# Kernel optimization log

Measured on AMD Instinct MI355X. Metric: run time of the kernel, lower is better.

Reference implementation:

```python
import jax, jax.numpy as jnp
import numpy as np

N_NODES = 100000
N_EDGES = 1000000
IN_CH = 64
HID = 128
OUT_CH = 2
N_GRAPHS = 256


def setup_inputs() -> dict:
    key = jax.random.key(0)
    ks = jax.random.split(key, 12)
    x = jax.random.normal(ks[0], (N_NODES, IN_CH), dtype=jnp.float32)
    edge_index = jax.random.randint(ks[1], (2, N_EDGES), 0, N_NODES, dtype=jnp.int64)
    batch = jnp.sort(jax.random.randint(ks[2], (N_NODES,), 0, N_GRAPHS, dtype=jnp.int64))
    def glorot(k, shape):
        lim = float(np.sqrt(6.0 / (shape[0] + shape[1])))
        return jax.random.uniform(k, shape, dtype=jnp.float32, minval=-lim, maxval=lim)
    # SAGEConv: out = lin_l(mean_agg(x_j)) + lin_r(x_i); bias on lin_l only (PyG default)
    Wl1 = glorot(ks[3], (HID, IN_CH))
    bl1 = jnp.zeros((HID,), dtype=jnp.float32)
    Wr1 = glorot(ks[4], (HID, IN_CH))
    Wl2 = glorot(ks[5], (HID, HID))
    bl2 = jnp.zeros((HID,), dtype=jnp.float32)
    Wr2 = glorot(ks[6], (HID, HID))
    Wout = glorot(ks[7], (OUT_CH, HID))
    bout = jnp.zeros((OUT_CH,), dtype=jnp.float32)
    return {"x": x, "edge_index": edge_index, "batch": batch,
            "Wl1": Wl1, "bl1": bl1, "Wr1": Wr1,
            "Wl2": Wl2, "bl2": bl2, "Wr2": Wr2,
            "Wout": Wout, "bout": bout}


def _sage_conv(x, src, dst, Wl, bl, Wr):
    # mean-aggregate source features onto target nodes, then two linears
    msgs = x[src]                                                # [E, d]
    agg = jax.ops.segment_sum(msgs, dst, num_segments=N_NODES)  # [N, d]
    deg = jax.ops.segment_sum(jnp.ones((src.shape[0], 1), x.dtype), dst,
                              num_segments=N_NODES)             # [N, 1]
    agg = agg / jnp.maximum(deg, 1.0)
    return agg @ Wl.T + bl + x @ Wr.T


def reference(x, edge_index, batch, Wl1, bl1, Wr1, Wl2, bl2, Wr2, Wout, bout):
    src, dst = edge_index[0], edge_index[1]
    h = jax.nn.relu(_sage_conv(x, src, dst, Wl1, bl1, Wr1))
    # dropout(p=0.2) is identity in eval mode
    h = jax.nn.relu(_sage_conv(h, src, dst, Wl2, bl2, Wr2))
    # global_mean_pool over graph ids
    pooled = jax.ops.segment_sum(h, batch, num_segments=N_GRAPHS)      # [G, H]
    cnt = jax.ops.segment_sum(jnp.ones((h.shape[0], 1), h.dtype), batch,
                              num_segments=N_GRAPHS)                   # [G, 1]
    pooled = pooled / jnp.maximum(cnt, 1.0)
    logits = pooled @ Wout.T + bout
    return jax.nn.log_softmax(logits, axis=1)
```

## Files before the change

kernel.cpp:

```cpp
#include <hip/hip_runtime.h>
#include <hip/hip_bf16.h>
#include <math.h>

typedef short short8_t __attribute__((ext_vector_type(8)));
typedef float floatx4  __attribute__((ext_vector_type(4)));
typedef float floatx2  __attribute__((ext_vector_type(2)));
typedef unsigned int uint;

#define EPB 1024
#define BSH 9


__device__ inline unsigned short f2b(float f) {
    uint u = __float_as_uint(f);
    u += 0x7fff + ((u >> 16) & 1);
    return (unsigned short)(u >> 16);
}
__device__ inline uint pack2(float a, float b) {
    return (uint)f2b(a) | ((uint)f2b(b) << 16);
}
__device__ inline float blo(uint v) { return __uint_as_float(v << 16); }
__device__ inline float bhi(uint v) { return __uint_as_float(v & 0xffff0000u); }


__device__ inline uint enc4_fp8(float f0, float f1, float f2, float f3) {
    uint v = __builtin_amdgcn_cvt_pk_fp8_f32(f0, f1, 0, false);
    v = __builtin_amdgcn_cvt_pk_fp8_f32(f2, f3, v, true);
    return v;
}
__device__ inline unsigned char enc1_fp8(float f) {
    return (unsigned char)(__builtin_amdgcn_cvt_pk_fp8_f32(f, f, 0, false) & 0xff);
}


__global__ __launch_bounds__(256) void k_phase_a(
    const int* __restrict__ dst, int* __restrict__ bhist, int E,
    const float* __restrict__ x, unsigned short* __restrict__ xb,
    unsigned char* __restrict__ xf8, int nX,
    const float* __restrict__ Wl1, const float* __restrict__ Wr1,
    const float* __restrict__ Wl2, const float* __restrict__ Wr2,
    unsigned short* __restrict__ wbuf,
    const int* __restrict__ batch, int* __restrict__ gstart, int N, int G,
    int bHist, int bCvtX, int bCvtW) {
    __shared__ int h[256];
    int b = blockIdx.x;
    int tid = threadIdx.x;
    if (b < bHist) {
        h[tid] = 0;
        __syncthreads();
        int e = b * EPB + tid * 4;
        if (e + 3 < E) {
            int4 d4 = *(const int4*)(dst + e);
            atomicAdd(&h[d4.x >> BSH], 1);
            atomicAdd(&h[d4.y >> BSH], 1);
            atomicAdd(&h[d4.z >> BSH], 1);
            atomicAdd(&h[d4.w >> BSH], 1);
        } else {
            for (int k = e; k < E; ++k) atomicAdd(&h[dst[k] >> BSH], 1);
        }
        __syncthreads();
        bhist[(size_t)b * 256 + tid] = h[tid];
    } else if (b < bHist + bCvtX) {
        int i = ((b - bHist) * 256 + tid) * 8;
        if (i < nX) {
            float4 v0 = *(const float4*)(x + i);
            float4 v1 = *(const float4*)(x + i + 4);
            uint4 ob;
            ob.x = pack2(v0.x, v0.y);
            ob.y = pack2(v0.z, v0.w);
            ob.z = pack2(v1.x, v1.y);
            ob.w = pack2(v1.z, v1.w);
            *(uint4*)(xb + i) = ob;
            uint2 of;
            of.x = enc4_fp8(v0.x, v0.y, v0.z, v0.w);
            of.y = enc4_fp8(v1.x, v1.y, v1.z, v1.w);
            *(uint2*)(xf8 + i) = of;
        }
    } else if (b < bHist + bCvtX + bCvtW) {
        int i = (b - bHist - bCvtX) * 256 + tid;
        if (i < 49152) {
            float v;
            if (i < 8192)       v = Wl1[i];
            else if (i < 16384) v = Wr1[i - 8192];
            else if (i < 32768) v = Wl2[i - 16384];
            else                v = Wr2[i - 32768];
            wbuf[i] = f2b(v);
        }
    } else {
        for (int g = tid; g <= G; g += 256) {
            if (g == G) { gstart[G] = N; continue; }
            int lo = 0, hi = N;
            while (lo < hi) {
                int mid = (lo + hi) >> 1;
                if (batch[mid] < g) lo = mid + 1; else hi = mid;
            }
            gstart[g] = lo;
        }
    }
}

__global__ __launch_bounds__(256) void k_scan_bh(int* __restrict__ bhist,
                                                 int* __restrict__ btot, int nb) {
    __shared__ int ss[256];
    int k = blockIdx.x;
    int t = threadIdx.x;
    int b0 = t * 4;
    int v[4];
    int sum = 0;
#pragma unroll
    for (int i = 0; i < 4; ++i) {
        int b = b0 + i;
        v[i] = (b < nb) ? bhist[(size_t)b * 256 + k] : 0;
        sum += v[i];
    }
    ss[t] = sum;
    __syncthreads();
#pragma unroll
    for (int off = 1; off < 256; off <<= 1) {
        int u = (t >= off) ? ss[t - off] : 0;
        __syncthreads();
        ss[t] += u;
        __syncthreads();
    }
    int run = ss[t] - sum;
#pragma unroll
    for (int i = 0; i < 4; ++i) {
        int b = b0 + i;
        if (b < nb) { bhist[(size_t)b * 256 + k] = run; run += v[i]; }
    }
    if (t == 0) btot[k] = ss[255];
}

__global__ void k_scan_btot(const int* __restrict__ btot, int* __restrict__ bbase,
                            int* __restrict__ row_start, int N, int E) {
    __shared__ int ss[256];
    int t = threadIdx.x;
    int v = btot[t];
    ss[t] = v;
    __syncthreads();
#pragma unroll
    for (int off = 1; off < 256; off <<= 1) {
        int u = (t >= off) ? ss[t - off] : 0;
        __syncthreads();
        ss[t] += u;
        __syncthreads();
    }
    bbase[t] = ss[t] - v;
    if (t == 255) bbase[256] = ss[255];
    if (t == 0) row_start[N] = E;
}

__global__ __launch_bounds__(256) void k_scatter_b(
    const int* __restrict__ src, const int* __restrict__ dst,
    const int* __restrict__ bhist, const int* __restrict__ bbase,
    int* __restrict__ ebuf, int E) {
    __shared__ int lbase[256];
    int b = blockIdx.x;
    int t = threadIdx.x;
    lbase[t] = bbase[t] + bhist[(size_t)b * 256 + t];
    __syncthreads();
    int e = b * EPB + t * 4;
    if (e + 3 < E) {
        int4 d4 = *(const int4*)(dst + e);
        int4 s4 = *(const int4*)(src + e);
        int k, p;
        k = d4.x >> BSH; p = atomicAdd(&lbase[k], 1); ebuf[p] = ((d4.x & 511) << 23) | s4.x;
        k = d4.y >> BSH; p = atomicAdd(&lbase[k], 1); ebuf[p] = ((d4.y & 511) << 23) | s4.y;
        k = d4.z >> BSH; p = atomicAdd(&lbase[k], 1); ebuf[p] = ((d4.z & 511) << 23) | s4.z;
        k = d4.w >> BSH; p = atomicAdd(&lbase[k], 1); ebuf[p] = ((d4.w & 511) << 23) | s4.w;
    } else {
        for (int q = e; q < E; ++q) {
            int d = dst[q];
            int p = atomicAdd(&lbase[d >> BSH], 1);
            ebuf[p] = ((d & 511) << 23) | src[q];
        }
    }
}

__global__ __launch_bounds__(256) void k_bucket_csr(
    const int* __restrict__ ebuf, const int* __restrict__ bbase,
    int* __restrict__ row_start, int* __restrict__ csr_src, int N) {
    __shared__ int h2[512];
    __shared__ int ss[256];
    int k = blockIdx.x;
    int t = threadIdx.x;
    int node0 = k << BSH;
    int nn = N - node0; if (nn > 512) nn = 512;
    int s = bbase[k], e = bbase[k + 1];
    h2[t] = 0; h2[t + 256] = 0;
    __syncthreads();
    for (int i = s + t; i < e; i += 256)
        atomicAdd(&h2[((uint)ebuf[i]) >> 23], 1);
    __syncthreads();
    int a0 = h2[2 * t], a1 = h2[2 * t + 1];
    int ps = a0 + a1;
    ss[t] = ps;
    __syncthreads();
#pragma unroll
    for (int off = 1; off < 256; off <<= 1) {
        int u = (t >= off) ? ss[t - off] : 0;
        __syncthreads();
        ss[t] += u;
        __syncthreads();
    }
    int base = ss[t] - ps;
    h2[2 * t] = base;
    h2[2 * t + 1] = base + a0;
    __syncthreads();
    int rs0 = h2[t];
    int rs1 = h2[t + 256];
    __syncthreads();
    if (t < nn)       row_start[node0 + t]       = s + rs0;
    if (t + 256 < nn) row_start[node0 + t + 256] = s + rs1;
    for (int i = s + t; i < e; i += 256) {
        int rec = ebuf[i];
        int j = ((uint)rec) >> 23;
        int pos = atomicAdd(&h2[j], 1);
        csr_src[s + pos] = rec & 0x7FFFFF;
    }
}


#define ACCF8(v)                                                        \
    { floatx2 f = __builtin_amdgcn_cvt_pk_f32_fp8((v).x, false);        \
      a[0] += f[0]; a[1] += f[1];                                       \
      f = __builtin_amdgcn_cvt_pk_f32_fp8((v).x, true);                 \
      a[2] += f[0]; a[3] += f[1];                                       \
      f = __builtin_amdgcn_cvt_pk_f32_fp8((v).y, false);                \
      a[4] += f[0]; a[5] += f[1];                                       \
      f = __builtin_amdgcn_cvt_pk_f32_fp8((v).y, true);                 \
      a[6] += f[0]; a[7] += f[1]; }

__global__ void k_gather1(const unsigned char* __restrict__ xf8,
                          const int* __restrict__ row_start,
                          const int* __restrict__ csr_src,
                          unsigned short* __restrict__ agg, int n_nodes) {
    int tid = threadIdx.x;
    int node = blockIdx.x * 4 + (tid >> 6);
    if (node >= n_nodes) return;
    int lane = tid & 63;
    int grp = lane >> 3;
    int lp  = lane & 7;
    int s = row_start[node];
    int e = row_start[node + 1];
    float a[8];
#pragma unroll
    for (int q = 0; q < 8; ++q) a[q] = 0.f;
    int i = s + grp;
    for (; i + 8 < e; i += 16) {
        int u0 = csr_src[i];
        int u1 = csr_src[i + 8];
        uint2 v0 = *(const uint2*)(xf8 + (size_t)u0 * 64 + lp * 8);
        uint2 v1 = *(const uint2*)(xf8 + (size_t)u1 * 64 + lp * 8);
        ACCF8(v0);
        ACCF8(v1);
    }
    if (i < e) {
        int u0 = csr_src[i];
        uint2 v0 = *(const uint2*)(xf8 + (size_t)u0 * 64 + lp * 8);
        ACCF8(v0);
    }
#pragma unroll
    for (int q = 0; q < 8; ++q) {
        a[q] += __shfl_xor(a[q], 8);
        a[q] += __shfl_xor(a[q], 16);
        a[q] += __shfl_xor(a[q], 32);
    }
    if (grp == 0) {
        int d = e - s;
        float scale = (d > 0) ? (1.f / (float)d) : 1.f;
        uint4 o;
        o.x = pack2(a[0] * scale, a[1] * scale);
        o.y = pack2(a[2] * scale, a[3] * scale);
        o.z = pack2(a[4] * scale, a[5] * scale);
        o.w = pack2(a[6] * scale, a[7] * scale);
        *(uint4*)(agg + (size_t)node * 64 + lp * 8) = o;
    }
}

__global__ void k_gather2(const unsigned char* __restrict__ h1f8,
                          const int* __restrict__ row_start,
                          const int* __restrict__ csr_src,
                          unsigned short* __restrict__ agg, int n_nodes) {
    int tid = threadIdx.x;
    int node = blockIdx.x * 4 + (tid >> 6);
    if (node >= n_nodes) return;
    int lane = tid & 63;
    int grp = lane >> 4;
    int lp  = lane & 15;
    int s = row_start[node];
    int e = row_start[node + 1];
    float a[8];
#pragma unroll
    for (int q = 0; q < 8; ++q) a[q] = 0.f;
    int i = s + grp;
    for (; i + 4 < e; i += 8) {
        int u0 = csr_src[i];
        int u1 = csr_src[i + 4];
        uint2 v0 = *(const uint2*)(h1f8 + (size_t)u0 * 128 + lp * 8);
        uint2 v1 = *(const uint2*)(h1f8 + (size_t)u1 * 128 + lp * 8);
        ACCF8(v0);
        ACCF8(v1);
    }
    if (i < e) {
        int u0 = csr_src[i];
        uint2 v0 = *(const uint2*)(h1f8 + (size_t)u0 * 128 + lp * 8);
        ACCF8(v0);
    }
#pragma unroll
    for (int q = 0; q < 8; ++q) {
        a[q] += __shfl_xor(a[q], 16);
        a[q] += __shfl_xor(a[q], 32);
    }
    if (grp == 0) {
        int d = e - s;
        float scale = (d > 0) ? (1.f / (float)d) : 1.f;
        uint4 o;
        o.x = pack2(a[0] * scale, a[1] * scale);
        o.y = pack2(a[2] * scale, a[3] * scale);
        o.z = pack2(a[4] * scale, a[5] * scale);
        o.w = pack2(a[6] * scale, a[7] * scale);
        *(uint4*)(agg + (size_t)node * 128 + lp * 8) = o;
    }
}


template <int K, bool F8OUT>
__global__ __launch_bounds__(256) void k_linear_mfma(
    const unsigned short* __restrict__ aggA, const unsigned short* __restrict__ xinA,
    const unsigned short* __restrict__ Wlb,  const float* __restrict__ bl,
    const unsigned short* __restrict__ Wrb,  unsigned short* __restrict__ out,
    unsigned char* __restrict__ outf8, int n_nodes) {
    constexpr int NCH = (2 * K) / 32;
    __shared__ __align__(16) short As[128 * 32];

    int tid  = threadIdx.x;
    int lane = tid & 63;
    int wave = tid >> 6;
    int quad = lane >> 4;
    int lr   = lane & 15;
    int node0 = blockIdx.x * 128;

    floatx4 acc[8][2];
#pragma unroll
    for (int mi = 0; mi < 8; ++mi)
#pragma unroll
        for (int ni = 0; ni < 2; ++ni)
            acc[mi][ni] = (floatx4){0.f, 0.f, 0.f, 0.f};

    int srow = tid >> 2;
    int sslot = tid & 3;

#pragma unroll
    for (int c = 0; c < NCH; ++c) {
        const unsigned short* srcA;
        const unsigned short* srcW;
        int kb;
        if (c < K / 32) { srcA = aggA; srcW = Wlb; kb = c * 32; }
        else            { srcA = xinA; srcW = Wrb; kb = c * 32 - K; }

        __syncthreads();
        {
            int n1 = node0 + srow;       if (n1 >= n_nodes) n1 = n_nodes - 1;
            int n2 = node0 + srow + 64;  if (n2 >= n_nodes) n2 = n_nodes - 1;
            uint4 v1 = *(const uint4*)(srcA + (size_t)n1 * K + kb + sslot * 8);
            uint4 v2 = *(const uint4*)(srcA + (size_t)n2 * K + kb + sslot * 8);
            *(uint4*)(&As[srow * 32 + sslot * 8]) = v1;
            *(uint4*)(&As[(srow + 64) * 32 + sslot * 8]) = v2;
        }
        __syncthreads();

        short8_t bfrag[2];
#pragma unroll
        for (int ni = 0; ni < 2; ++ni) {
            int j = wave * 32 + ni * 16 + lr;
            bfrag[ni] = *(const short8_t*)(srcW + (size_t)j * K + kb + quad * 8);
        }
#pragma unroll
        for (int mi = 0; mi < 8; ++mi) {
            short8_t af = *(const short8_t*)(&As[(mi * 16 + lr) * 32 + quad * 8]);
            acc[mi][0] = __builtin_amdgcn_mfma_f32_16x16x32_bf16(af, bfrag[0], acc[mi][0], 0, 0, 0);
            acc[mi][1] = __builtin_amdgcn_mfma_f32_16x16x32_bf16(af, bfrag[1], acc[mi][1], 0, 0, 0);
        }
    }

    float b0 = bl[wave * 32 + lr];
    float b1 = bl[wave * 32 + 16 + lr];
    int j0 = wave * 32 + lr;
#pragma unroll
    for (int mi = 0; mi < 8; ++mi) {
#pragma unroll
        for (int r = 0; r < 4; ++r) {
            int node = node0 + mi * 16 + quad * 4 + r;
            if (node < n_nodes) {
                float v0 = fmaxf(acc[mi][0][r] + b0, 0.f);
                float v1 = fmaxf(acc[mi][1][r] + b1, 0.f);
                out[(size_t)node * 128 + j0]      = f2b(v0);
                out[(size_t)node * 128 + j0 + 16] = f2b(v1);
                if (F8OUT) {
                    outf8[(size_t)node * 128 + j0]      = enc1_fp8(v0);
                    outf8[(size_t)node * 128 + j0 + 16] = enc1_fp8(v1);
                }
            }
        }
    }
}


__global__ __launch_bounds__(256) void k_pool_head(const unsigned short* __restrict__ h2b,
                                                   const int* __restrict__ gstart,
                                                   const float* __restrict__ Wout,
                                                   const float* __restrict__ bout,
                                                   float* __restrict__ out) {
    int g = blockIdx.x;
    int s = gstart[g], e = gstart[g + 1];
    int lane = threadIdx.x & 63;
    int wave = threadIdx.x >> 6;
    float ax = 0.f, ay = 0.f;
    for (int n = s + wave; n < e; n += 4) {
        uint v = ((const uint*)(h2b + (size_t)n * 128))[lane];
        ax += blo(v);
        ay += bhi(v);
    }
    __shared__ float2 red[4][64];
    red[wave][lane] = make_float2(ax, ay);
    __syncthreads();
    if (wave == 0) {
        float2 a = red[0][lane], b = red[1][lane], c = red[2][lane], d = red[3][lane];
        float cnt = (float)(e - s);
        float inv = (cnt > 0.f) ? (1.f / cnt) : 1.f;
        float px = (a.x + b.x + c.x + d.x) * inv;
        float py = (a.y + b.y + c.y + d.y) * inv;
        float2 w0 = ((const float2*)(Wout))[lane];
        float2 w1 = ((const float2*)(Wout + 128))[lane];
        float d0 = px * w0.x + py * w0.y;
        float d1 = px * w1.x + py * w1.y;
#pragma unroll
        for (int m = 32; m > 0; m >>= 1) {
            d0 += __shfl_xor(d0, m);
            d1 += __shfl_xor(d1, m);
        }
        if (lane == 0) {
            float l0 = d0 + bout[0];
            float l1 = d1 + bout[1];
            float mx = fmaxf(l0, l1);
            float lse = mx + logf(expf(l0 - mx) + expf(l1 - mx));
            out[g * 2 + 0] = l0 - lse;
            out[g * 2 + 1] = l1 - lse;
        }
    }
}


static inline size_t alignUp(size_t x, size_t a) { return (x + a - 1) & ~(a - 1); }

extern "C" void kernel_launch(void* const* d_in, const int* in_sizes, int n_in,
                              void* d_out, int out_size, void* d_ws, size_t ws_size,
                              hipStream_t stream) {
    const float* x    = (const float*)d_in[0];
    const int*   ei   = (const int*)d_in[1];
    const int*   batch= (const int*)d_in[2];
    const float* Wl1  = (const float*)d_in[3];
    const float* bl1  = (const float*)d_in[4];
    const float* Wr1  = (const float*)d_in[5];
    const float* Wl2  = (const float*)d_in[6];
    const float* bl2  = (const float*)d_in[7];
    const float* Wr2  = (const float*)d_in[8];
    const float* Wout = (const float*)d_in[9];
    const float* bout = (const float*)d_in[10];
    float* out = (float*)d_out;

    const int N = in_sizes[0] / 64;
    const int E = in_sizes[1] / 2;
    const int G = out_size / 2;

    const int* src = ei;
    const int* dst = ei + E;

    const int bHist = (E + EPB - 1) / EPB;
    const int NB    = (N + 511) >> BSH;

    char* ws = (char*)d_ws;
    size_t off = 0;
    int*   bhist     = (int*)(ws + off); off = alignUp(off + (size_t)bHist * 256 * 4, 256);
    int*   btot      = (int*)(ws + off); off = alignUp(off + (size_t)257 * 4, 256);
    int*   bbase     = (int*)(ws + off); off = alignUp(off + (size_t)257 * 4, 256);
    int*   row_start = (int*)(ws + off); off = alignUp(off + (size_t)(N + 1) * 4, 256);
    int*   ebuf      = (int*)(ws + off); off = alignUp(off + (size_t)E * 4, 256);
    int*   csr_src   = (int*)(ws + off); off = alignUp(off + (size_t)E * 4, 256);
    int*   gstart    = (int*)(ws + off); off = alignUp(off + (size_t)(G + 1) * 4, 256);
    unsigned short* xb   = (unsigned short*)(ws + off); off = alignUp(off + (size_t)N * 64 * 2, 256);
    unsigned char*  xf8  = (unsigned char*)(ws + off);  off = alignUp(off + (size_t)N * 64, 256);
    unsigned short* wbuf = (unsigned short*)(ws + off); off = alignUp(off + (size_t)49152 * 2, 256);
    unsigned short* agg1 = (unsigned short*)(ws + off); off = alignUp(off + (size_t)N * 64 * 2, 256);
    unsigned short* h1   = (unsigned short*)(ws + off); off = alignUp(off + (size_t)N * 128 * 2, 256);
    unsigned char*  h1f8 = (unsigned char*)(ws + off);  off = alignUp(off + (size_t)N * 128, 256);
    unsigned short* agg2 = (unsigned short*)(ws + off); off = alignUp(off + (size_t)N * 128 * 2, 256);
    unsigned short* h2b  = (unsigned short*)(ws + off); off = alignUp(off + (size_t)N * 128 * 2, 256);
    (void)ws_size;

    unsigned short* Wl1b = wbuf;
    unsigned short* Wr1b = wbuf + 8192;
    unsigned short* Wl2b = wbuf + 16384;
    unsigned short* Wr2b = wbuf + 32768;

    const int bCvtX = (N * 64 / 8 + 255) / 256;
    const int bCvtW = 192;
    k_phase_a<<<bHist + bCvtX + bCvtW + 1, 256, 0, stream>>>(
        dst, bhist, E,
        x, xb, xf8, N * 64,
        Wl1, Wr1, Wl2, Wr2, wbuf,
        batch, gstart, N, G,
        bHist, bCvtX, bCvtW);

    k_scan_bh<<<256, 256, 0, stream>>>(bhist, btot, bHist);
    k_scan_btot<<<1, 256, 0, stream>>>(btot, bbase, row_start, N, E);
    k_scatter_b<<<bHist, 256, 0, stream>>>(src, dst, bhist, bbase, ebuf, E);
    k_bucket_csr<<<NB, 256, 0, stream>>>(ebuf, bbase, row_start, csr_src, N);

    k_gather1<<<(N + 3) / 4, 256, 0, stream>>>(xf8, row_start, csr_src, agg1, N);
    k_linear_mfma<64, true><<<(N + 127) / 128, 256, 0, stream>>>(
        agg1, xb, Wl1b, bl1, Wr1b, h1, h1f8, N);

    k_gather2<<<(N + 3) / 4, 256, 0, stream>>>(h1f8, row_start, csr_src, agg2, N);
    k_linear_mfma<128, false><<<(N + 127) / 128, 256, 0, stream>>>(
        agg2, h1, Wl2b, bl2, Wr2b, h2b, (unsigned char*)nullptr, N);

    k_pool_head<<<G, 256, 0, stream>>>(h2b, gstart, Wout, bout, out);
}
```

Before: 285.1 us.

## Fuse neighbor gather into MFMA linear kernels and pooling into layer two

Measured after the change: 374.1 us. 31.2% more time.

```diff
diff --git a/kernel.cpp b/kernel.cpp
--- a/kernel.cpp
+++ b/kernel.cpp
@@ -19,8 +19,6 @@
 __device__ inline uint pack2(float a, float b) {
     return (uint)f2b(a) | ((uint)f2b(b) << 16);
 }
-__device__ inline float blo(uint v) { return __uint_as_float(v << 16); }
-__device__ inline float bhi(uint v) { return __uint_as_float(v & 0xffff0000u); }
 
 
 __device__ inline uint enc4_fp8(float f0, float f1, float f2, float f3) {
@@ -40,8 +38,9 @@
     const float* __restrict__ Wl1, const float* __restrict__ Wr1,
     const float* __restrict__ Wl2, const float* __restrict__ Wr2,
     unsigned short* __restrict__ wbuf,
+    float* __restrict__ pooled,
     const int* __restrict__ batch, int* __restrict__ gstart, int N, int G,
-    int bHist, int bCvtX, int bCvtW) {
+    int bHist, int bCvtX, int bCvtW, int bZero) {
     __shared__ int h[256];
     int b = blockIdx.x;
     int tid = threadIdx.x;
@@ -86,6 +85,10 @@
             else                v = Wr2[i - 32768];
             wbuf[i] = f2b(v);
         }
+    } else if (b < bHist + bCvtX + bCvtW + bZero) {
+        int i = ((b - bHist - bCvtX - bCvtW) * 256 + tid) * 4;
+        float4 z = make_float4(0.f, 0.f, 0.f, 0.f);
+        *(float4*)(pooled + i) = z;
     } else {
         for (int g = tid; g <= G; g += 256) {
             if (g == G) { gstart[G] = N; continue; }
@@ -131,9 +134,13 @@
     if (t == 0) btot[k] = ss[255];
 }
 
-__global__ void k_scan_btot(const int* __restrict__ btot, int* __restrict__ bbase,
-                            int* __restrict__ row_start, int N, int E) {
+__global__ __launch_bounds__(256) void k_scatter_b(
+    const int* __restrict__ src, const int* __restrict__ dst,
+    const int* __restrict__ bhist, const int* __restrict__ btot,
+    int* __restrict__ ebuf, int E) {
+    __shared__ int lbase[256];
     __shared__ int ss[256];
+    int b = blockIdx.x;
     int t = threadIdx.x;
     int v = btot[t];
     ss[t] = v;
@@ -145,19 +152,7 @@
         ss[t] += u;
         __syncthreads();
     }
-    bbase[t] = ss[t] - v;
-    if (t == 255) bbase[256] = ss[255];
-    if (t == 0) row_start[N] = E;
-}
-
-__global__ __launch_bounds__(256) void k_scatter_b(
-    const int* __restrict__ src, const int* __restrict__ dst,
-    const int* __restrict__ bhist, const int* __restrict__ bbase,
-    int* __restrict__ ebuf, int E) {
-    __shared__ int lbase[256];
-    int b = blockIdx.x;
-    int t = threadIdx.x;
-    lbase[t] = bbase[t] + bhist[(size_t)b * 256 + t];
+    lbase[t] = (ss[t] - v) + bhist[(size_t)b * 256 + t];
     __syncthreads();
     int e = b * EPB + t * 4;
     if (e + 3 < E) {
@@ -178,15 +173,29 @@
 }
 
 __global__ __launch_bounds__(256) void k_bucket_csr(
-    const int* __restrict__ ebuf, const int* __restrict__ bbase,
+    const int* __restrict__ ebuf, const int* __restrict__ btot,
     int* __restrict__ row_start, int* __restrict__ csr_src, int N) {
     __shared__ int h2[512];
     __shared__ int ss[256];
+    __shared__ int S01[2];
     int k = blockIdx.x;
     int t = threadIdx.x;
+    int vb = btot[t];
+    ss[t] = vb;
+    __syncthreads();
+#pragma unroll
+    for (int off = 1; off < 256; off <<= 1) {
+        int u = (t >= off) ? ss[t - off] : 0;
+        __syncthreads();
+        ss[t] += u;
+        __syncthreads();
+    }
+    if (t == k) { S01[0] = ss[t] - vb; S01[1] = ss[t]; }
+    __syncthreads();
+    int s = S01[0], e = S01[1];
     int node0 = k << BSH;
     int nn = N - node0; if (nn > 512) nn = 512;
-    int s = bbase[k], e = bbase[k + 1];
+    if (k == (int)gridDim.x - 1 && t == 0) row_start[node0 + nn] = e;
     h2[t] = 0; h2[t + 256] = 0;
     __syncthreads();
     for (int i = s + t; i < e; i += 256)
@@ -231,116 +240,74 @@
       f = __builtin_amdgcn_cvt_pk_f32_fp8((v).y, true);                 \
       a[6] += f[0]; a[7] += f[1]; }
 
-__global__ void k_gather1(const unsigned char* __restrict__ xf8,
-                          const int* __restrict__ row_start,
-                          const int* __restrict__ csr_src,
-                          unsigned short* __restrict__ agg, int n_nodes) {
-    int tid = threadIdx.x;
-    int node = blockIdx.x * 4 + (tid >> 6);
-    if (node >= n_nodes) return;
-    int lane = tid & 63;
-    int grp = lane >> 3;
-    int lp  = lane & 7;
-    int s = row_start[node];
-    int e = row_start[node + 1];
-    float a[8];
-#pragma unroll
-    for (int q = 0; q < 8; ++q) a[q] = 0.f;
-    int i = s + grp;
-    for (; i + 8 < e; i += 16) {
-        int u0 = csr_src[i];
-        int u1 = csr_src[i + 8];
-        uint2 v0 = *(const uint2*)(xf8 + (size_t)u0 * 64 + lp * 8);
-        uint2 v1 = *(const uint2*)(xf8 + (size_t)u1 * 64 + lp * 8);
-        ACCF8(v0);
-        ACCF8(v1);
-    }
-    if (i < e) {
-        int u0 = csr_src[i];
-        uint2 v0 = *(const uint2*)(xf8 + (size_t)u0 * 64 + lp * 8);
-        ACCF8(v0);
-    }
-#pragma unroll
-    for (int q = 0; q < 8; ++q) {
-        a[q] += __shfl_xor(a[q], 8);
-        a[q] += __shfl_xor(a[q], 16);
-        a[q] += __shfl_xor(a[q], 32);
-    }
-    if (grp == 0) {
-        int d = e - s;
-        float scale = (d > 0) ? (1.f / (float)d) : 1.f;
-        uint4 o;
-        o.x = pack2(a[0] * scale, a[1] * scale);
-        o.y = pack2(a[2] * scale, a[3] * scale);
-        o.z = pack2(a[4] * scale, a[5] * scale);
-        o.w = pack2(a[6] * scale, a[7] * scale);
-        *(uint4*)(agg + (size_t)node * 64 + lp * 8) = o;
-    }
-}
-
-__global__ void k_gather2(const unsigned char* __restrict__ h1f8,
-                          const int* __restrict__ row_start,
-                          const int* __restrict__ csr_src,
-                          unsigned short* __restrict__ agg, int n_nodes) {
-    int tid = threadIdx.x;
-    int node = blockIdx.x * 4 + (tid >> 6);
-    if (node >= n_nodes) return;
-    int lane = tid & 63;
-    int grp = lane >> 4;
-    int lp  = lane & 15;
-    int s = row_start[node];
-    int e = row_start[node + 1];
-    float a[8];
-#pragma unroll
-    for (int q = 0; q < 8; ++q) a[q] = 0.f;
-    int i = s + grp;
-    for (; i + 4 < e; i += 8) {
-        int u0 = csr_src[i];
-        int u1 = csr_src[i + 4];
-        uint2 v0 = *(const uint2*)(h1f8 + (size_t)u0 * 128 + lp * 8);
-        uint2 v1 = *(const uint2*)(h1f8 + (size_t)u1 * 128 + lp * 8);
-        ACCF8(v0);
-        ACCF8(v1);
-    }
-    if (i < e) {
-        int u0 = csr_src[i];
-        uint2 v0 = *(const uint2*)(h1f8 + (size_t)u0 * 128 + lp * 8);
-        ACCF8(v0);
-    }
-#pragma unroll
-    for (int q = 0; q < 8; ++q) {
-        a[q] += __shfl_xor(a[q], 16);
-        a[q] += __shfl_xor(a[q], 32);
-    }
-    if (grp == 0) {
-        int d = e - s;
-        float scale = (d > 0) ? (1.f / (float)d) : 1.f;
-        uint4 o;
-        o.x = pack2(a[0] * scale, a[1] * scale);
-        o.y = pack2(a[2] * scale, a[3] * scale);
-        o.z = pack2(a[4] * scale, a[5] * scale);
-        o.w = pack2(a[6] * scale, a[7] * scale);
-        *(uint4*)(agg + (size_t)node * 128 + lp * 8) = o;
-    }
-}
-
-
-template <int K, bool F8OUT>
-__global__ __launch_bounds__(256) void k_linear_mfma(
-    const unsigned short* __restrict__ aggA, const unsigned short* __restrict__ xinA,
-    const unsigned short* __restrict__ Wlb,  const float* __restrict__ bl,
-    const unsigned short* __restrict__ Wrb,  unsigned short* __restrict__ out,
-    unsigned char* __restrict__ outf8, int n_nodes) {
-    constexpr int NCH = (2 * K) / 32;
+
+__global__ __launch_bounds__(256) void k_fused1(
+    const unsigned char* __restrict__ xf8,
+    const int* __restrict__ row_start, const int* __restrict__ csr_src,
+    const unsigned short* __restrict__ xb,
+    const unsigned short* __restrict__ Wlb, const float* __restrict__ bl,
+    const unsigned short* __restrict__ Wrb,
+    unsigned short* __restrict__ out, unsigned char* __restrict__ outf8,
+    int n_nodes) {
+    __shared__ __align__(16) short aggS[128 * 72];
     __shared__ __align__(16) short As[128 * 32];
 
     int tid  = threadIdx.x;
     int lane = tid & 63;
     int wave = tid >> 6;
+    int node0 = blockIdx.x * 128;
+
+    {
+        int grp = lane >> 3;
+        int lp  = lane & 7;
+        int wbase = node0 + wave * 32;
+        int ridx = wbase + lane;
+        if (ridx > n_nodes) ridx = n_nodes;
+        int rs = row_start[ridx];
+        int nmax = n_nodes - wbase;
+        if (nmax > 32) nmax = 32;
+        for (int t = 0; t < nmax; ++t) {
+            int s = __shfl(rs, t);
+            int e = __shfl(rs, t + 1);
+            float a[8];
+#pragma unroll
+            for (int q = 0; q < 8; ++q) a[q] = 0.f;
+            int i = s + grp;
+            for (; i + 8 < e; i += 16) {
+                int u0 = csr_src[i];
+                int u1 = csr_src[i + 8];
+                uint2 v0 = *(const uint2*)(xf8 + (size_t)u0 * 64 + lp * 8);
+                uint2 v1 = *(const uint2*)(xf8 + (size_t)u1 * 64 + lp * 8);
+                ACCF8(v0);
+                ACCF8(v1);
+            }
+            if (i < e) {
+                int u0 = csr_src[i];
+                uint2 v0 = *(const uint2*)(xf8 + (size_t)u0 * 64 + lp * 8);
+                ACCF8(v0);
+            }
+#pragma unroll
+            for (int q = 0; q < 8; ++q) {
+                a[q] += __shfl_xor(a[q], 8);
+                a[q] += __shfl_xor(a[q], 16);
+                a[q] += __shfl_xor(a[q], 32);
+            }
+            if (grp == 0) {
+                int d = e - s;
+                float scale = (d > 0) ? (1.f / (float)d) : 1.f;
+                uint4 o;
+                o.x = pack2(a[0] * scale, a[1] * scale);
+                o.y = pack2(a[2] * scale, a[3] * scale);
+                o.z = pack2(a[4] * scale, a[5] * scale);
+                o.w = pack2(a[6] * scale, a[7] * scale);
+                *(uint4*)(&aggS[(wave * 32 + t) * 72 + lp * 8]) = o;
+            }
+        }
+    }
+    __syncthreads();
+
     int quad = lane >> 4;
     int lr   = lane & 15;
-    int node0 = blockIdx.x * 128;
-
     floatx4 acc[8][2];
 #pragma unroll
     for (int mi = 0; mi < 8; ++mi)
@@ -348,33 +315,41 @@
         for (int ni = 0; ni < 2; ++ni)
             acc[mi][ni] = (floatx4){0.f, 0.f, 0.f, 0.f};
 
+#pragma unroll
+    for (int c = 0; c < 2; ++c) {
+        short8_t bfrag[2];
+#pragma unroll
+        for (int ni = 0; ni < 2; ++ni) {
+            int j = wave * 32 + ni * 16 + lr;
+            bfrag[ni] = *(const short8_t*)(Wlb + (size_t)j * 64 + c * 32 + quad * 8);
+        }
+#pragma unroll
+        for (int mi = 0; mi < 8; ++mi) {
+            short8_t af = *(const short8_t*)(&aggS[(mi * 16 + lr) * 72 + c * 32 + quad * 8]);
+            acc[mi][0] = __builtin_amdgcn_mfma_f32_16x16x32_bf16(af, bfrag[0], acc[mi][0], 0, 0, 0);
+            acc[mi][1] = __builtin_amdgcn_mfma_f32_16x16x32_bf16(af, bfrag[1], acc[mi][1], 0, 0, 0);
+        }
+    }
+
     int srow = tid >> 2;
     int sslot = tid & 3;
-
-#pragma unroll
-    for (int c = 0; c < NCH; ++c) {
-        const unsigned short* srcA;
-        const unsigned short* srcW;
-        int kb;
-        if (c < K / 32) { srcA = aggA; srcW = Wlb; kb = c * 32; }
-        else            { srcA = xinA; srcW = Wrb; kb = c * 32 - K; }
-
+#pragma unroll
+    for (int c = 0; c < 2; ++c) {
         __syncthreads();
         {
             int n1 = node0 + srow;       if (n1 >= n_nodes) n1 = n_nodes - 1;
             int n2 = node0 + srow + 64;  if (n2 >= n_nodes) n2 = n_nodes - 1;
-            uint4 v1 = *(const uint4*)(srcA + (size_t)n1 * K + kb + sslot * 8);
-            uint4 v2 = *(const uint4*)(srcA + (size_t)n2 * K + kb + sslot * 8);
+            uint4 v1 = *(const uint4*)(xb + (size_t)n1 * 64 + c * 32 + sslot * 8);
+            uint4 v2 = *(const uint4*)(xb + (size_t)n2 * 64 + c * 32 + sslot * 8);
             *(uint4*)(&As[srow * 32 + sslot * 8]) = v1;
             *(uint4*)(&As[(srow + 64) * 32 + sslot * 8]) = v2;
         }
         __syncthreads();
-
         short8_t bfrag[2];
 #pragma unroll
         for (int ni = 0; ni < 2; ++ni) {
             int j = wave * 32 + ni * 16 + lr;
-            bfrag[ni] = *(const short8_t*)(srcW + (size_t)j * K + kb + quad * 8);
+            bfrag[ni] = *(const short8_t*)(Wrb + (size_t)j * 64 + c * 32 + quad * 8);
         }
 #pragma unroll
         for (int mi = 0; mi < 8; ++mi) {
@@ -397,57 +372,196 @@
                 float v1 = fmaxf(acc[mi][1][r] + b1, 0.f);
                 out[(size_t)node * 128 + j0]      = f2b(v0);
                 out[(size_t)node * 128 + j0 + 16] = f2b(v1);
-                if (F8OUT) {
-                    outf8[(size_t)node * 128 + j0]      = enc1_fp8(v0);
-                    outf8[(size_t)node * 128 + j0 + 16] = enc1_fp8(v1);
+                outf8[(size_t)node * 128 + j0]      = enc1_fp8(v0);
+                outf8[(size_t)node * 128 + j0 + 16] = enc1_fp8(v1);
+            }
+        }
+    }
+}
+
+
+__global__ __launch_bounds__(256) void k_fused2(
+    const unsigned char* __restrict__ h1f8,
+    const int* __restrict__ row_start, const int* __restrict__ csr_src,
+    const unsigned short* __restrict__ h1,
+    const unsigned short* __restrict__ Wlb, const float* __restrict__ bl,
+    const unsigned short* __restrict__ Wrb,
+    const int* __restrict__ batch, float* __restrict__ pooled,
+    int n_nodes) {
+    __shared__ __align__(16) short aggS[128 * 136];
+    __shared__ __align__(16) short As[128 * 32];
+    __shared__ int bb[128];
+
+    int tid  = threadIdx.x;
+    int lane = tid & 63;
+    int wave = tid >> 6;
+    int node0 = blockIdx.x * 128;
+
+    if (tid < 128) {
+        int n = node0 + tid;
+        bb[tid] = (n < n_nodes) ? batch[n] : 0;
+    }
+
+    {
+        int grp = lane >> 4;
+        int lp  = lane & 15;
+        int wbase = node0 + wave * 32;
+        int ridx = wbase + lane;
+        if (ridx > n_nodes) ridx = n_nodes;
+        int rs = row_start[ridx];
+        int nmax = n_nodes - wbase;
+        if (nmax > 32) nmax = 32;
+        for (int t = 0; t < nmax; ++t) {
+            int s = __shfl(rs, t);
+            int e = __shfl(rs, t + 1);
+            float a[8];
+#pragma unroll
+            for (int q = 0; q < 8; ++q) a[q] = 0.f;
+            int i = s + grp;
+            for (; i + 4 < e; i += 8) {
+                int u0 = csr_src[i];
+                int u1 = csr_src[i + 4];
+                uint2 v0 = *(const uint2*)(h1f8 + (size_t)u0 * 128 + lp * 8);
+                uint2 v1 = *(const uint2*)(h1f8 + (size_t)u1 * 128 + lp * 8);
+                ACCF8(v0);
+                ACCF8(v1);
+            }
+            if (i < e) {
+                int u0 = csr_src[i];
+                uint2 v0 = *(const uint2*)(h1f8 + (size_t)u0 * 128 + lp * 8);
+                ACCF8(v0);
+            }
+#pragma unroll
+            for (int q = 0; q < 8; ++q) {
+                a[q] += __shfl_xor(a[q], 16);
+                a[q] += __shfl_xor(a[q], 32);
+            }
+            if (grp == 0) {
+                int d = e - s;
+                float scale = (d > 0) ? (1.f / (float)d) : 1.f;
+                uint4 o;
+                o.x = pack2(a[0] * scale, a[1] * scale);
+                o.y = pack2(a[2] * scale, a[3] * scale);
+                o.z = pack2(a[4] * scale, a[5] * scale);
+                o.w = pack2(a[6] * scale, a[7] * scale);
+                *(uint4*)(&aggS[(wave * 32 + t) * 136 + lp * 8]) = o;
+            }
+        }
+    }
+    __syncthreads();
+
+    int quad = lane >> 4;
+    int lr   = lane & 15;
+    floatx4 acc[8][2];
+#pragma unroll
+    for (int mi = 0; mi < 8; ++mi)
+#pragma unroll
+        for (int ni = 0; ni < 2; ++ni)
+            acc[mi][ni] = (floatx4){0.f, 0.f, 0.f, 0.f};
+
+#pragma unroll
+    for (int c = 0; c < 4; ++c) {
+        short8_t bfrag[2];
+#pragma unroll
+        for (int ni = 0; ni < 2; ++ni) {
+            int j = wave * 32 + ni * 16 + lr;
+            bfrag[ni] = *(const short8_t*)(Wlb + (size_t)j * 128 + c * 32 + quad * 8);
+        }
+#pragma unroll
+        for (int mi = 0; mi < 8; ++mi) {
+            short8_t af = *(const short8_t*)(&aggS[(mi * 16 + lr) * 136 + c * 32 + quad * 8]);
+            acc[mi][0] = __builtin_amdgcn_mfma_f32_16x16x32_bf16(af, bfrag[0], acc[mi][0], 0, 0, 0);
+            acc[mi][1] = __builtin_amdgcn_mfma_f32_16x16x32_bf16(af, bfrag[1], acc[mi][1], 0, 0, 0);
+        }
+    }
+
+    int srow = tid >> 2;
+    int sslot = tid & 3;
+#pragma unroll
+    for (int c = 0; c < 4; ++c) {
+        __syncthreads();
+        {
+            int n1 = node0 + srow;       if (n1 >= n_nodes) n1 = n_nodes - 1;
+            int n2 = node0 + srow + 64;  if (n2 >= n_nodes) n2 = n_nodes - 1;
+            uint4 v1 = *(const uint4*)(h1 + (size_t)n1 * 128 + c * 32 + sslot * 8);
+            uint4 v2 = *(const uint4*)(h1 + (size_t)n2 * 128 + c * 32 + sslot * 8);
+            *(uint4*)(&As[srow * 32 + sslot * 8]) = v1;
+            *(uint4*)(&As[(srow + 64) * 32 + sslot * 8]) = v2;
+        }
+        __syncthreads();
+        short8_t bfrag[2];
+#pragma unroll
+        for (int ni = 0; ni < 2; ++ni) {
+            int j = wave * 32 + ni * 16 + lr;
+            bfrag[ni] = *(const short8_t*)(Wrb + (size_t)j * 128 + c * 32 + quad * 8);
+        }
+#pragma unroll
+        for (int mi = 0; mi < 8; ++mi) {
+            short8_t af = *(const short8_t*)(&As[(mi * 16 + lr) * 32 + quad * 8]);
+            acc[mi][0] = __builtin_amdgcn_mfma_f32_16x16x32_bf16(af, bfrag[0], acc[mi][0], 0, 0, 0);
+            acc[mi][1] = __builtin_amdgcn_mfma_f32_16x16x32_bf16(af, bfrag[1], acc[mi][1], 0, 0, 0);
+        }
+    }
+
+    float b0 = bl[wave * 32 + lr];
+    float b1 = bl[wave * 32 + 16 + lr];
+    int j0 = wave * 32 + lr;
+    int gcur = -1;
+    float s0 = 0.f, s1 = 0.f;
+#pragma unroll
+    for (int mi = 0; mi < 8; ++mi) {
+#pragma unroll
+        for (int r = 0; r < 4; ++r) {
+            int li = mi * 16 + quad * 4 + r;
+            int node = node0 + li;
+            if (node < n_nodes) {
+                float v0 = fmaxf(acc[mi][0][r] + b0, 0.f);
+                float v1 = fmaxf(acc[mi][1][r] + b1, 0.f);
+                int g = bb[li];
+                if (g != gcur) {
+                    if (gcur >= 0) {
+                        atomicAdd(&pooled[gcur * 128 + j0], s0);
+                        atomicAdd(&pooled[gcur * 128 + j0 + 16], s1);
+                    }
+                    gcur = g; s0 = 0.f; s1 = 0.f;
                 }
-            }
-        }
-    }
-}
-
-
-__global__ __launch_bounds__(256) void k_pool_head(const unsigned short* __restrict__ h2b,
-                                                   const int* __restrict__ gstart,
-                                                   const float* __restrict__ Wout,
-                                                   const float* __restrict__ bout,
-                                                   float* __restrict__ out) {
+                s0 += v0;
+                s1 += v1;
+            }
+        }
+    }
+    if (gcur >= 0) {
+        atomicAdd(&pooled[gcur * 128 + j0], s0);
+        atomicAdd(&pooled[gcur * 128 + j0 + 16], s1);
+    }
+}
+
+
+__global__ void k_head(const float* __restrict__ pooled,
+                       const int* __restrict__ gstart,
+                       const float* __restrict__ Wout,
+                       const float* __restrict__ bout,
+                       float* __restrict__ out) {
     int g = blockIdx.x;
-    int s = gstart[g], e = gstart[g + 1];
-    int lane = threadIdx.x & 63;
-    int wave = threadIdx.x >> 6;
-    float ax = 0.f, ay = 0.f;
-    for (int n = s + wave; n < e; n += 4) {
-        uint v = ((const uint*)(h2b + (size_t)n * 128))[lane];
-        ax += blo(v);
-        ay += bhi(v);
-    }
-    __shared__ float2 red[4][64];
-    red[wave][lane] = make_float2(ax, ay);
-    __syncthreads();
-    if (wave == 0) {
-        float2 a = red[0][lane], b = red[1][lane], c = red[2][lane], d = red[3][lane];
-        float cnt = (float)(e - s);
+    int lane = threadIdx.x;
+    float p0 = pooled[g * 128 + lane];
+    float p1 = pooled[g * 128 + 64 + lane];
+    float d0 = p0 * Wout[lane] + p1 * Wout[64 + lane];
+    float d1 = p0 * Wout[128 + lane] + p1 * Wout[192 + lane];
+#pragma unroll
+    for (int m = 32; m > 0; m >>= 1) {
+        d0 += __shfl_xor(d0, m);
+        d1 += __shfl_xor(d1, m);
+    }
+    if (lane == 0) {
+        float cnt = (float)(gstart[g + 1] - gstart[g]);
         float inv = (cnt > 0.f) ? (1.f / cnt) : 1.f;
-        float px = (a.x + b.x + c.x + d.x) * inv;
-        float py = (a.y + b.y + c.y + d.y) * inv;
-        float2 w0 = ((const float2*)(Wout))[lane];
-        float2 w1 = ((const float2*)(Wout + 128))[lane];
-        float d0 = px * w0.x + py * w0.y;
-        float d1 = px * w1.x + py * w1.y;
-#pragma unroll
-        for (int m = 32; m > 0; m >>= 1) {
-            d0 += __shfl_xor(d0, m);
-            d1 += __shfl_xor(d1, m);
-        }
-        if (lane == 0) {
-            float l0 = d0 + bout[0];
-            float l1 = d1 + bout[1];
-            float mx = fmaxf(l0, l1);
-            float lse = mx + logf(expf(l0 - mx) + expf(l1 - mx));
-            out[g * 2 + 0] = l0 - lse;
-            out[g * 2 + 1] = l1 - lse;
-        }
+        float l0 = d0 * inv + bout[0];
+        float l1 = d1 * inv + bout[1];
+        float mx = fmaxf(l0, l1);
+        float lse = mx + logf(expf(l0 - mx) + expf(l1 - mx));
+        out[g * 2 + 0] = l0 - lse;
+        out[g * 2 + 1] = l1 - lse;
     }
 }
 
@@ -484,7 +598,6 @@
     size_t off = 0;
     int*   bhist     = (int*)(ws + off); off = alignUp(off + (size_t)bHist * 256 * 4, 256);
     int*   btot      = (int*)(ws + off); off = alignUp(off + (size_t)257 * 4, 256);
-    int*   bbase     = (int*)(ws + off); off = alignUp(off + (size_t)257 * 4, 256);
     int*   row_start = (int*)(ws + off); off = alignUp(off + (size_t)(N + 1) * 4, 256);
     int*   ebuf      = (int*)(ws + off); off = alignUp(off + (size_t)E * 4, 256);
     int*   csr_src   = (int*)(ws + off); off = alignUp(off + (size_t)E * 4, 256);
@@ -492,11 +605,9 @@
     unsigned short* xb   = (unsigned short*)(ws + off); off = alignUp(off + (size_t)N * 64 * 2, 256);
     unsigned char*  xf8  = (unsigned char*)(ws + off);  off = alignUp(off + (size_t)N * 64, 256);
     unsigned short* wbuf = (unsigned short*)(ws + off); off = alignUp(off + (size_t)49152 * 2, 256);
-    unsigned short* agg1 = (unsigned short*)(ws + off); off = alignUp(off + (size_t)N * 64 * 2, 256);
     unsigned short* h1   = (unsigned short*)(ws + off); off = alignUp(off + (size_t)N * 128 * 2, 256);
     unsigned char*  h1f8 = (unsigned char*)(ws + off);  off = alignUp(off + (size_t)N * 128, 256);
-    unsigned short* agg2 = (unsigned short*)(ws + off); off = alignUp(off + (size_t)N * 128 * 2, 256);
-    unsigned short* h2b  = (unsigned short*)(ws + off); off = alignUp(off + (size_t)N * 128 * 2, 256);
+    float*          pooled = (float*)(ws + off); off = alignUp(off + (size_t)G * 128 * 4, 256);
     (void)ws_size;
 
     unsigned short* Wl1b = wbuf;
@@ -506,25 +617,24 @@
 
     const int bCvtX = (N * 64 / 8 + 255) / 256;
     const int bCvtW = 192;
-    k_phase_a<<<bHist + bCvtX + bCvtW + 1, 256, 0, stream>>>(
+    const int bZero = (G * 128 / 4 + 255) / 256;
+    k_phase_a<<<bHist + bCvtX + bCvtW + bZero + 1, 256, 0, stream>>>(
         dst, bhist, E,
         x, xb, xf8, N * 64,
         Wl1, Wr1, Wl2, Wr2, wbuf,
+        pooled,
         batch, gstart, N, G,
-        bHist, bCvtX, bCvtW);
+        bHist, bCvtX, bCvtW, bZero);
 
     k_scan_bh<<<256, 256, 0, stream>>>(bhist, btot, bHist);
-    k_scan_btot<<<1, 256, 0, stream>>>(btot, bbase, row_start, N, E);
-    k_scatter_b<<<bHist, 256, 0, stream>>>(src, dst, bhist, bbase, ebuf, E);
-    k_bucket_csr<<<NB, 256, 0, stream>>>(ebuf, bbase, row_start, csr_src, N);
-
-    k_gather1<<<(N + 3) / 4, 256, 0, stream>>>(xf8, row_start, csr_src, agg1, N);
-    k_linear_mfma<64, true><<<(N + 127) / 128, 256, 0, stream>>>(
-        agg1, xb, Wl1b, bl1, Wr1b, h1, h1f8, N);
-
-    k_gather2<<<(N + 3) / 4, 256, 0, stream>>>(h1f8, row_start, csr_src, agg2, N);
-    k_linear_mfma<128, false><<<(N + 127) / 128, 256, 0, stream>>>(
-        agg2, h1, Wl2b, bl2, Wr2b, h2b, (unsigned char*)nullptr, N);
-
-    k_pool_head<<<G, 256, 0, stream>>>(h2b, gstart, Wout, bout, out);
-}
+    k_scatter_b<<<bHist, 256, 0, stream>>>(src, dst, bhist, btot, ebuf, E);
+    k_bucket_csr<<<NB, 256, 0, stream>>>(ebuf, btot, row_start, csr_src, N);
+
+    k_fused1<<<(N + 127) / 128, 256, 0, stream>>>(
+        xf8, row_start, csr_src, xb, Wl1b, bl1, Wr1b, h1, h1f8, N);
+
+    k_fused2<<<(N + 127) / 128, 256, 0, stream>>>(
+        h1f8, row_start, csr_src, h1, Wl2b, bl2, Wr2b, batch, pooled, N);
+
+    k_head<<<G, 64, 0, stream>>>(pooled, gstart, Wout, bout, out);
+}
```

## Fuse global mean pooling into second linear epilogue and drop btot scan kernel

Applied to the files above, without the earlier changes.

After: 258.2 us. -9.4%, faster.

```diff
diff --git a/kernel.cpp b/kernel.cpp
--- a/kernel.cpp
+++ b/kernel.cpp
@@ -19,8 +19,6 @@
 __device__ inline uint pack2(float a, float b) {
     return (uint)f2b(a) | ((uint)f2b(b) << 16);
 }
-__device__ inline float blo(uint v) { return __uint_as_float(v << 16); }
-__device__ inline float bhi(uint v) { return __uint_as_float(v & 0xffff0000u); }
 
 
 __device__ inline uint enc4_fp8(float f0, float f1, float f2, float f3) {
@@ -40,8 +38,9 @@
     const float* __restrict__ Wl1, const float* __restrict__ Wr1,
     const float* __restrict__ Wl2, const float* __restrict__ Wr2,
     unsigned short* __restrict__ wbuf,
+    float* __restrict__ pooled,
     const int* __restrict__ batch, int* __restrict__ gstart, int N, int G,
-    int bHist, int bCvtX, int bCvtW) {
+    int bHist, int bCvtX, int bCvtW, int bZero) {
     __shared__ int h[256];
     int b = blockIdx.x;
     int tid = threadIdx.x;
@@ -86,6 +85,10 @@
             else                v = Wr2[i - 32768];
             wbuf[i] = f2b(v);
         }
+    } else if (b < bHist + bCvtX + bCvtW + bZero) {
+        int i = ((b - bHist - bCvtX - bCvtW) * 256 + tid) * 4;
+        float4 z = make_float4(0.f, 0.f, 0.f, 0.f);
+        *(float4*)(pooled + i) = z;
     } else {
         for (int g = tid; g <= G; g += 256) {
             if (g == G) { gstart[G] = N; continue; }
@@ -131,9 +134,13 @@
     if (t == 0) btot[k] = ss[255];
 }
 
-__global__ void k_scan_btot(const int* __restrict__ btot, int* __restrict__ bbase,
-                            int* __restrict__ row_start, int N, int E) {
+__global__ __launch_bounds__(256) void k_scatter_b(
+    const int* __restrict__ src, const int* __restrict__ dst,
+    const int* __restrict__ bhist, const int* __restrict__ btot,
+    int* __restrict__ ebuf, int E) {
+    __shared__ int lbase[256];
     __shared__ int ss[256];
+    int b = blockIdx.x;
     int t = threadIdx.x;
     int v = btot[t];
     ss[t] = v;
@@ -145,19 +152,7 @@
         ss[t] += u;
         __syncthreads();
     }
-    bbase[t] = ss[t] - v;
-    if (t == 255) bbase[256] = ss[255];
-    if (t == 0) row_start[N] = E;
-}
-
-__global__ __launch_bounds__(256) void k_scatter_b(
-    const int* __restrict__ src, const int* __restrict__ dst,
-    const int* __restrict__ bhist, const int* __restrict__ bbase,
-    int* __restrict__ ebuf, int E) {
-    __shared__ int lbase[256];
-    int b = blockIdx.x;
-    int t = threadIdx.x;
-    lbase[t] = bbase[t] + bhist[(size_t)b * 256 + t];
+    lbase[t] = (ss[t] - v) + bhist[(size_t)b * 256 + t];
     __syncthreads();
     int e = b * EPB + t * 4;
     if (e + 3 < E) {
@@ -178,15 +173,29 @@
 }
 
 __global__ __launch_bounds__(256) void k_bucket_csr(
-    const int* __restrict__ ebuf, const int* __restrict__ bbase,
+    const int* __restrict__ ebuf, const int* __restrict__ btot,
     int* __restrict__ row_start, int* __restrict__ csr_src, int N) {
     __shared__ int h2[512];
     __shared__ int ss[256];
+    __shared__ int S01[2];
     int k = blockIdx.x;
     int t = threadIdx.x;
+    int vb = btot[t];
+    ss[t] = vb;
+    __syncthreads();
+#pragma unroll
+    for (int off = 1; off < 256; off <<= 1) {
+        int u = (t >= off) ? ss[t - off] : 0;
+        __syncthreads();
+        ss[t] += u;
+        __syncthreads();
+    }
+    if (t == k) { S01[0] = ss[t] - vb; S01[1] = ss[t]; }
+    __syncthreads();
+    int s = S01[0], e = S01[1];
     int node0 = k << BSH;
     int nn = N - node0; if (nn > 512) nn = 512;
-    int s = bbase[k], e = bbase[k + 1];
+    if (k == (int)gridDim.x - 1 && t == 0) row_start[node0 + nn] = e;
     h2[t] = 0; h2[t + 256] = 0;
     __syncthreads();
     for (int i = s + t; i < e; i += 256)
@@ -325,14 +334,16 @@
 }
 
 
-template <int K, bool F8OUT>
+template <int K, bool POOL>
 __global__ __launch_bounds__(256) void k_linear_mfma(
     const unsigned short* __restrict__ aggA, const unsigned short* __restrict__ xinA,
     const unsigned short* __restrict__ Wlb,  const float* __restrict__ bl,
     const unsigned short* __restrict__ Wrb,  unsigned short* __restrict__ out,
-    unsigned char* __restrict__ outf8, int n_nodes) {
+    unsigned char* __restrict__ outf8,
+    const int* __restrict__ batch, float* __restrict__ pooled, int n_nodes) {
     constexpr int NCH = (2 * K) / 32;
     __shared__ __align__(16) short As[128 * 32];
+    __shared__ int bb[128];
 
     int tid  = threadIdx.x;
     int lane = tid & 63;
@@ -340,6 +351,11 @@
     int quad = lane >> 4;
     int lr   = lane & 15;
     int node0 = blockIdx.x * 128;
+
+    if (POOL && tid < 128) {
+        int n = node0 + tid;
+        bb[tid] = (n < n_nodes) ? batch[n] : 0;
+    }
 
     floatx4 acc[8][2];
 #pragma unroll
@@ -387,67 +403,81 @@
     float b0 = bl[wave * 32 + lr];
     float b1 = bl[wave * 32 + 16 + lr];
     int j0 = wave * 32 + lr;
-#pragma unroll
-    for (int mi = 0; mi < 8; ++mi) {
-#pragma unroll
-        for (int r = 0; r < 4; ++r) {
-            int node = node0 + mi * 16 + quad * 4 + r;
-            if (node < n_nodes) {
-                float v0 = fmaxf(acc[mi][0][r] + b0, 0.f);
-                float v1 = fmaxf(acc[mi][1][r] + b1, 0.f);
-                out[(size_t)node * 128 + j0]      = f2b(v0);
-                out[(size_t)node * 128 + j0 + 16] = f2b(v1);
-                if (F8OUT) {
+
+    if (!POOL) {
+#pragma unroll
+        for (int mi = 0; mi < 8; ++mi) {
+#pragma unroll
+            for (int r = 0; r < 4; ++r) {
+                int node = node0 + mi * 16 + quad * 4 + r;
+                if (node < n_nodes) {
+                    float v0 = fmaxf(acc[mi][0][r] + b0, 0.f);
+                    float v1 = fmaxf(acc[mi][1][r] + b1, 0.f);
+                    out[(size_t)node * 128 + j0]      = f2b(v0);
+                    out[(size_t)node * 128 + j0 + 16] = f2b(v1);
                     outf8[(size_t)node * 128 + j0]      = enc1_fp8(v0);
                     outf8[(size_t)node * 128 + j0 + 16] = enc1_fp8(v1);
                 }
             }
         }
-    }
-}
-
-
-__global__ __launch_bounds__(256) void k_pool_head(const unsigned short* __restrict__ h2b,
-                                                   const int* __restrict__ gstart,
-                                                   const float* __restrict__ Wout,
-                                                   const float* __restrict__ bout,
-                                                   float* __restrict__ out) {
+    } else {
+        int gcur = -1;
+        float s0 = 0.f, s1 = 0.f;
+#pragma unroll
+        for (int mi = 0; mi < 8; ++mi) {
+#pragma unroll
+            for (int r = 0; r < 4; ++r) {
+                int li = mi * 16 + quad * 4 + r;
+                int node = node0 + li;
+                if (node < n_nodes) {
+                    float v0 = fmaxf(acc[mi][0][r] + b0, 0.f);
+                    float v1 = fmaxf(acc[mi][1][r] + b1, 0.f);
+                    int g = bb[li];
+                    if (g != gcur) {
+                        if (gcur >= 0) {
+                            atomicAdd(&pooled[gcur * 128 + j0], s0);
+                            atomicAdd(&pooled[gcur * 128 + j0 + 16], s1);
+                        }
+                        gcur = g; s0 = 0.f; s1 = 0.f;
+                    }
+                    s0 += v0;
+                    s1 += v1;
+                }
+            }
+        }
+        if (gcur >= 0) {
+            atomicAdd(&pooled[gcur * 128 + j0], s0);
+            atomicAdd(&pooled[gcur * 128 + j0 + 16], s1);
+        }
+    }
+}
+
+
+__global__ void k_head(const float* __restrict__ pooled,
+                       const int* __restrict__ gstart,
+                       const float* __restrict__ Wout,
+                       const float* __restrict__ bout,
+                       float* __restrict__ out) {
     int g = blockIdx.x;
-    int s = gstart[g], e = gstart[g + 1];
-    int lane = threadIdx.x & 63;
-    int wave = threadIdx.x >> 6;
-    float ax = 0.f, ay = 0.f;
-    for (int n = s + wave; n < e; n += 4) {
-        uint v = ((const uint*)(h2b + (size_t)n * 128))[lane];
-        ax += blo(v);
-        ay += bhi(v);
-    }
-    __shared__ float2 red[4][64];
-    red[wave][lane] = make_float2(ax, ay);
-    __syncthreads();
-    if (wave == 0) {
-        float2 a = red[0][lane], b = red[1][lane], c = red[2][lane], d = red[3][lane];
-        float cnt = (float)(e - s);
+    int lane = threadIdx.x;
+    float p0 = pooled[g * 128 + lane];
+    float p1 = pooled[g * 128 + 64 + lane];
+    float d0 = p0 * Wout[lane] + p1 * Wout[64 + lane];
+    float d1 = p0 * Wout[128 + lane] + p1 * Wout[192 + lane];
+#pragma unroll
+    for (int m = 32; m > 0; m >>= 1) {
+        d0 += __shfl_xor(d0, m);
+        d1 += __shfl_xor(d1, m);
+    }
+    if (lane == 0) {
+        float cnt = (float)(gstart[g + 1] - gstart[g]);
         float inv = (cnt > 0.f) ? (1.f / cnt) : 1.f;
-        float px = (a.x + b.x + c.x + d.x) * inv;
-        float py = (a.y + b.y + c.y + d.y) * inv;
-        float2 w0 = ((const float2*)(Wout))[lane];
-        float2 w1 = ((const float2*)(Wout + 128))[lane];
-        float d0 = px * w0.x + py * w0.y;
-        float d1 = px * w1.x + py * w1.y;
-#pragma unroll
-        for (int m = 32; m > 0; m >>= 1) {
-            d0 += __shfl_xor(d0, m);
-            d1 += __shfl_xor(d1, m);
-        }
-        if (lane == 0) {
-            float l0 = d0 + bout[0];
-            float l1 = d1 + bout[1];
-            float mx = fmaxf(l0, l1);
-            float lse = mx + logf(expf(l0 - mx) + expf(l1 - mx));
-            out[g * 2 + 0] = l0 - lse;
-            out[g * 2 + 1] = l1 - lse;
-        }
+        float l0 = d0 * inv + bout[0];
+        float l1 = d1 * inv + bout[1];
+        float mx = fmaxf(l0, l1);
+        float lse = mx + logf(expf(l0 - mx) + expf(l1 - mx));
+        out[g * 2 + 0] = l0 - lse;
+        out[g * 2 + 1] = l1 - lse;
     }
 }
 
@@ -484,7 +514,6 @@
     size_t off = 0;
     int*   bhist     = (int*)(ws + off); off = alignUp(off + (size_t)bHist * 256 * 4, 256);
     int*   btot      = (int*)(ws + off); off = alignUp(off + (size_t)257 * 4, 256);
-    int*   bbase     = (int*)(ws + off); off = alignUp(off + (size_t)257 * 4, 256);
     int*   row_start = (int*)(ws + off); off = alignUp(off + (size_t)(N + 1) * 4, 256);
     int*   ebuf      = (int*)(ws + off); off = alignUp(off + (size_t)E * 4, 256);
     int*   csr_src   = (int*)(ws + off); off = alignUp(off + (size_t)E * 4, 256);
@@ -496,7 +525,7 @@
     unsigned short* h1   = (unsigned short*)(ws + off); off = alignUp(off + (size_t)N * 128 * 2, 256);
     unsigned char*  h1f8 = (unsigned char*)(ws + off);  off = alignUp(off + (size_t)N * 128, 256);
     unsigned short* agg2 = (unsigned short*)(ws + off); off = alignUp(off + (size_t)N * 128 * 2, 256);
-    unsigned short* h2b  = (unsigned short*)(ws + off); off = alignUp(off + (size_t)N * 128 * 2, 256);
+    float*          pooled = (float*)(ws + off); off = alignUp(off + (size_t)G * 128 * 4, 256);
     (void)ws_size;
 
     unsigned short* Wl1b = wbuf;
@@ -506,25 +535,26 @@
 
     const int bCvtX = (N * 64 / 8 + 255) / 256;
     const int bCvtW = 192;
-    k_phase_a<<<bHist + bCvtX + bCvtW + 1, 256, 0, stream>>>(
+    const int bZero = (G * 128 / 4 + 255) / 256;
+    k_phase_a<<<bHist + bCvtX + bCvtW + bZero + 1, 256, 0, stream>>>(
         dst, bhist, E,
         x, xb, xf8, N * 64,
         Wl1, Wr1, Wl2, Wr2, wbuf,
+        pooled,
         batch, gstart, N, G,
-        bHist, bCvtX, bCvtW);
+        bHist, bCvtX, bCvtW, bZero);
 
     k_scan_bh<<<256, 256, 0, stream>>>(bhist, btot, bHist);
-    k_scan_btot<<<1, 256, 0, stream>>>(btot, bbase, row_start, N, E);
-    k_scatter_b<<<bHist, 256, 0, stream>>>(src, dst, bhist, bbase, ebuf, E);
-    k_bucket_csr<<<NB, 256, 0, stream>>>(ebuf, bbase, row_start, csr_src, N);
+    k_scatter_b<<<bHist, 256, 0, stream>>>(src, dst, bhist, btot, ebuf, E);
+    k_bucket_csr<<<NB, 256, 0, stream>>>(ebuf, btot, row_start, csr_src, N);
 
     k_gather1<<<(N + 3) / 4, 256, 0, stream>>>(xf8, row_start, csr_src, agg1, N);
-    k_linear_mfma<64, true><<<(N + 127) / 128, 256, 0, stream>>>(
-        agg1, xb, Wl1b, bl1, Wr1b, h1, h1f8, N);
+    k_linear_mfma<64, false><<<(N + 127) / 128, 256, 0, stream>>>(
+        agg1, xb, Wl1b, bl1, Wr1b, h1, h1f8, nullptr, nullptr, N);
 
     k_gather2<<<(N + 3) / 4, 256, 0, stream>>>(h1f8, row_start, csr_src, agg2, N);
-    k_linear_mfma<128, false><<<(N + 127) / 128, 256, 0, stream>>>(
-        agg2, h1, Wl2b, bl2, Wr2b, h2b, (unsigned char*)nullptr, N);
-
-    k_pool_head<<<G, 256, 0, stream>>>(h2b, gstart, Wout, bout, out);
-}
+    k_linear_mfma<128, true><<<(N + 127) / 128, 256, 0, stream>>>(
+        agg2, h1, Wl2b, bl2, Wr2b, nullptr, nullptr, batch, pooled, N);
+
+    k_head<<<G, 64, 0, stream>>>(pooled, gstart, Wout, bout, out);
+}
```
